# Kernel optimization log

Hardware: AMD Instinct MI355X
Metric: run time of the kernel (lower is better)

Reference implementation:

```python
import jax, jax.numpy as jnp
import numpy as np

N_NODES = 50000
N_EDGES = 800000
N_EVAL = 500000
D = 96


def _sage_conv(x, edge_index, W_l, W_r, b):
    # PyG SAGEConv with aggr='add':
    #   aggr_out[v] = sum_{(u->v) in edges} x[u]
    #   out = aggr_out @ W_l^T-equivalent + b + x @ W_r  (we store W as [in, out])
    src, dst = edge_index[0], edge_index[1]
    msgs = x[src]                                        # [E, d_in] irregular gather
    aggr = jax.ops.segment_sum(msgs, dst, num_segments=x.shape[0])  # [N, d_in]
    return aggr @ W_l + b + x @ W_r                      # [N, d_out]


def setup_inputs() -> dict:
    key = jax.random.key(0)
    ks = jax.random.split(key, 8)
    scale = 1.0 / np.sqrt(D)
    Features = jax.random.normal(ks[0], (N_NODES, D), dtype=jnp.float32)
    A = jax.random.randint(ks[1], (2, N_EDGES), 0, N_NODES, dtype=jnp.int64)
    E = jax.random.randint(ks[2], (2, N_EVAL), 0, N_NODES, dtype=jnp.int64)
    W1_l = jax.random.normal(ks[3], (D, D), dtype=jnp.float32) * scale
    W1_r = jax.random.normal(ks[4], (D, D), dtype=jnp.float32) * scale
    b1 = jnp.zeros((D,), dtype=jnp.float32)
    W2_l = jax.random.normal(ks[5], (D, D), dtype=jnp.float32) * scale
    W2_r = jax.random.normal(ks[6], (D, D), dtype=jnp.float32) * scale
    b2 = jnp.zeros((D,), dtype=jnp.float32)
    return {"Features": Features, "A": A, "E": E,
            "W1_l": W1_l, "W1_r": W1_r, "b1": b1,
            "W2_l": W2_l, "W2_r": W2_r, "b2": b2}


def reference(Features, A, E, W1_l, W1_r, b1, W2_l, W2_r, b2):
    h = _sage_conv(Features, A, W1_l, W1_r, b1)          # [N, hidden]
    h = jax.nn.relu(h)
    # dropout in eval mode = identity
    h = _sage_conv(h, A, W2_l, W2_r, b2)                 # [N, out]
    # edge scoring: gather src/dst embeddings, dot, sigmoid
    src = h[E[0]]                                        # [n_eval, out]
    dst = h[E[1]]                                        # [n_eval, out]
    return jax.nn.sigmoid(jnp.sum(src * dst, axis=-1))   # [n_eval]
```

## Files before the change

### kernel.cpp

```cpp
#include <hip/hip_runtime.h>
#include <math.h>

#define N_NODES 50000
#define N_EDGES 800000
#define N_EVAL  500000
#define SCAN_NB ((N_NODES + 1023) / 1024)
#define CSTRIDE 16

__device__ __forceinline__ float4 f4add(float4 a, float4 b) {
    return make_float4(a.x + b.x, a.y + b.y, a.z + b.z, a.w + b.w);
}
__device__ __forceinline__ float4 f4fma(float s, float4 w, float4 a) {
    return make_float4(fmaf(s, w.x, a.x), fmaf(s, w.y, a.y),
                       fmaf(s, w.z, a.z), fmaf(s, w.w, a.w));
}


__global__ __launch_bounds__(256) void k_rank(const int* __restrict__ dst,
                                              int* __restrict__ degS,
                                              int* __restrict__ rank) {
    int e = blockIdx.x * 256 + threadIdx.x;
    if (e < N_EDGES) {
        int d = dst[e];
        rank[e] = atomicAdd(&degS[(size_t)d * CSTRIDE], 1);
    }
}

__global__ __launch_bounds__(1024) void k_scan1(const int* __restrict__ degS,
                                                int* __restrict__ off,
                                                int* __restrict__ bsum) {
    __shared__ int wsum[16];
    const int idx  = blockIdx.x * 1024 + threadIdx.x;
    const int lane = threadIdx.x & 63;
    const int wid  = threadIdx.x >> 6;
    int v = (idx < N_NODES) ? degS[(size_t)idx * CSTRIDE] : 0;
    int s = v;
    #pragma unroll
    for (int d = 1; d < 64; d <<= 1) {
        int o = __shfl_up(s, (unsigned)d, 64);
        if (lane >= d) s += o;
    }
    if (lane == 63) wsum[wid] = s;
    __syncthreads();
    if (wid == 0) {
        int ws = (lane < 16) ? wsum[lane] : 0;
        #pragma unroll
        for (int d = 1; d < 16; d <<= 1) {
            int o = __shfl_up(ws, (unsigned)d, 64);
            if (lane >= d) ws += o;
        }
        if (lane < 16) wsum[lane] = ws;
    }
    __syncthreads();
    int incl = (wid ? wsum[wid - 1] : 0) + s;
    if (idx < N_NODES) off[idx] = incl - v;
    if (threadIdx.x == 1023) bsum[blockIdx.x] = incl;
}

__global__ __launch_bounds__(64) void k_scan2(int* __restrict__ bsum,
                                              int* __restrict__ off) {
    int lane = threadIdx.x;
    int v = (lane < SCAN_NB) ? bsum[lane] : 0;
    int s = v;
    #pragma unroll
    for (int d = 1; d < 64; d <<= 1) {
        int o = __shfl_up(s, (unsigned)d, 64);
        if (lane >= d) s += o;
    }
    if (lane < SCAN_NB) bsum[lane] = s - v;
    if (lane == 63) off[N_NODES] = s;
}

__global__ __launch_bounds__(1024) void k_scan3(const int* __restrict__ bsum,
                                                int* __restrict__ off) {
    int idx = blockIdx.x * 1024 + threadIdx.x;
    if (idx < N_NODES) off[idx] += bsum[blockIdx.x];
}

__global__ __launch_bounds__(256) void k_fill(const int* __restrict__ src,
                                              const int* __restrict__ dst,
                                              const int* __restrict__ rank,
                                              const int* __restrict__ off,
                                              int* __restrict__ csr) {
    int e = blockIdx.x * 256 + threadIdx.x;
    if (e < N_EDGES) {
        csr[off[dst[e]] + rank[e]] = src[e];
    }
}

__global__ __launch_bounds__(256) void k_aggr(const float* __restrict__ x,
                                              const int* __restrict__ off,
                                              const int* __restrict__ csr,
                                              float* __restrict__ out) {
    int gt = blockIdx.x * 256 + threadIdx.x;
    if (gt >= N_NODES * 24) return;
    int v = gt / 24;
    int c = gt - v * 24;
    const float* xp = x + c * 4;
    int beg = off[v], end = off[v + 1];
    float4 a0 = make_float4(0.f, 0.f, 0.f, 0.f);
    float4 a1 = make_float4(0.f, 0.f, 0.f, 0.f);
    int i = beg;
    for (; i + 8 <= end; i += 8) {
        int u0 = csr[i + 0], u1 = csr[i + 1], u2 = csr[i + 2], u3 = csr[i + 3];
        int u4 = csr[i + 4], u5 = csr[i + 5], u6 = csr[i + 6], u7 = csr[i + 7];
        float4 t0 = *(const float4*)(xp + (size_t)u0 * 96);
        float4 t1 = *(const float4*)(xp + (size_t)u1 * 96);
        float4 t2 = *(const float4*)(xp + (size_t)u2 * 96);
        float4 t3 = *(const float4*)(xp + (size_t)u3 * 96);
        float4 t4 = *(const float4*)(xp + (size_t)u4 * 96);
        float4 t5 = *(const float4*)(xp + (size_t)u5 * 96);
        float4 t6 = *(const float4*)(xp + (size_t)u6 * 96);
        float4 t7 = *(const float4*)(xp + (size_t)u7 * 96);
        a0 = f4add(a0, f4add(f4add(t0, t2), f4add(t4, t6)));
        a1 = f4add(a1, f4add(f4add(t1, t3), f4add(t5, t7)));
    }
    for (; i < end; ++i) {
        int u = csr[i];
        a0 = f4add(a0, *(const float4*)(xp + (size_t)u * 96));
    }
    *(float4*)(out + (size_t)v * 96 + c * 4) = f4add(a0, a1);
}

template <int RELU>
__global__ __launch_bounds__(192) void k_gemm(const float* __restrict__ P,
                                              const float* __restrict__ X,
                                              const float* __restrict__ Wl,
                                              const float* __restrict__ Wr,
                                              const float* __restrict__ bias,
                                              float* __restrict__ out) {
    __shared__ float Ws[32 * 96];
    __shared__ float xT[32 * 68];
    const int tid = threadIdx.x;
    const int q   = tid % 24;
    const int rg  = tid / 24;
    const int v0  = blockIdx.x * 64;

    const int  row0 = tid >> 3,         qd0 = tid & 7;
    const int  row1 = (tid + 192) >> 3, qd1 = (tid + 192) & 7;
    const int  row2 = (tid + 384) >> 3, qd2 = (tid + 384) & 7;
    const bool has2 = (tid < 128);
    int sv0 = v0 + row0; if (sv0 >= N_NODES) sv0 = N_NODES - 1;
    int sv1 = v0 + row1; if (sv1 >= N_NODES) sv1 = N_NODES - 1;
    int sv2 = v0 + row2; if (sv2 >= N_NODES) sv2 = N_NODES - 1;

    float4 bv = *(const float4*)(bias + q * 4);
    float4 acc[8];
    #pragma unroll
    for (int r = 0; r < 8; ++r) acc[r] = make_float4(0.f, 0.f, 0.f, 0.f);

    float4 wreg0, wreg1, wreg2, wreg3;
    float4 xreg0, xreg1, xreg2;

    auto load_chunk = [&](int kc) {
        const float* W = (kc < 3 ? Wl : Wr) + (kc % 3) * (32 * 96);
        const float* M = (kc < 3 ? P : X);
        const int kbase = (kc % 3) * 32;
        wreg0 = *(const float4*)(W + (tid + 0 * 192) * 4);
        wreg1 = *(const float4*)(W + (tid + 1 * 192) * 4);
        wreg2 = *(const float4*)(W + (tid + 2 * 192) * 4);
        wreg3 = *(const float4*)(W + (tid + 3 * 192) * 4);
        xreg0 = *(const float4*)(M + (size_t)sv0 * 96 + kbase + qd0 * 4);
        xreg1 = *(const float4*)(M + (size_t)sv1 * 96 + kbase + qd1 * 4);
        if (has2) xreg2 = *(const float4*)(M + (size_t)sv2 * 96 + kbase + qd2 * 4);
    };
    auto store_chunk = [&]() {
        *(float4*)(Ws + (tid + 0 * 192) * 4) = wreg0;
        *(float4*)(Ws + (tid + 1 * 192) * 4) = wreg1;
        *(float4*)(Ws + (tid + 2 * 192) * 4) = wreg2;
        *(float4*)(Ws + (tid + 3 * 192) * 4) = wreg3;
        int k0 = qd0 * 4;
        xT[(k0 + 0) * 68 + row0] = xreg0.x;
        xT[(k0 + 1) * 68 + row0] = xreg0.y;
        xT[(k0 + 2) * 68 + row0] = xreg0.z;
        xT[(k0 + 3) * 68 + row0] = xreg0.w;
        int k1 = qd1 * 4;
        xT[(k1 + 0) * 68 + row1] = xreg1.x;
        xT[(k1 + 1) * 68 + row1] = xreg1.y;
        xT[(k1 + 2) * 68 + row1] = xreg1.z;
        xT[(k1 + 3) * 68 + row1] = xreg1.w;
        if (has2) {
            int k2 = qd2 * 4;
            xT[(k2 + 0) * 68 + row2] = xreg2.x;
            xT[(k2 + 1) * 68 + row2] = xreg2.y;
            xT[(k2 + 2) * 68 + row2] = xreg2.z;
            xT[(k2 + 3) * 68 + row2] = xreg2.w;
        }
    };

    load_chunk(0);
    for (int kc = 0; kc < 6; ++kc) {
        __syncthreads();
        store_chunk();
        if (kc < 5) load_chunk(kc + 1);
        __syncthreads();
        #pragma unroll 8
        for (int kk = 0; kk < 32; ++kk) {
            float4 w  = *(const float4*)(Ws + kk * 96 + q * 4);
            float4 xa = *(const float4*)(xT + kk * 68 + rg * 8);
            float4 xb = *(const float4*)(xT + kk * 68 + rg * 8 + 4);
            acc[0] = f4fma(xa.x, w, acc[0]);
            acc[1] = f4fma(xa.y, w, acc[1]);
            acc[2] = f4fma(xa.z, w, acc[2]);
            acc[3] = f4fma(xa.w, w, acc[3]);
            acc[4] = f4fma(xb.x, w, acc[4]);
            acc[5] = f4fma(xb.y, w, acc[5]);
            acc[6] = f4fma(xb.z, w, acc[6]);
            acc[7] = f4fma(xb.w, w, acc[7]);
        }
    }
    #pragma unroll
    for (int r = 0; r < 8; ++r) {
        int v = v0 + rg * 8 + r;
        if (v < N_NODES) {
            float4 o = f4add(acc[r], bv);
            if (RELU) {
                o.x = fmaxf(o.x, 0.f); o.y = fmaxf(o.y, 0.f);
                o.z = fmaxf(o.z, 0.f); o.w = fmaxf(o.w, 0.f);
            }
            *(float4*)(out + (size_t)v * 96 + q * 4) = o;
        }
    }
}

__global__ __launch_bounds__(256) void k_score(const float* __restrict__ h,
                                               const int* __restrict__ E,
                                               float* __restrict__ out) {
    int t = blockIdx.x * 256 + threadIdx.x;
    int e = t >> 3, sub = t & 7;
    if (e >= N_EVAL) return;
    int s = E[e];
    int d = E[N_EVAL + e];
    const float* ps = h + (size_t)s * 96 + sub * 12;
    const float* pd = h + (size_t)d * 96 + sub * 12;
    float dot = 0.f;
    #pragma unroll
    for (int i = 0; i < 3; ++i) {
        float4 a = *(const float4*)(ps + i * 4);
        float4 b = *(const float4*)(pd + i * 4);
        dot += a.x * b.x + a.y * b.y + a.z * b.z + a.w * b.w;
    }
    dot += __shfl_xor(dot, 1, 64);
    dot += __shfl_xor(dot, 2, 64);
    dot += __shfl_xor(dot, 4, 64);
    if (sub == 0) out[e] = 1.f / (1.f + expf(-dot));
}


extern "C" void kernel_launch(void* const* d_in, const int* in_sizes, int n_in,
                              void* d_out, int out_size, void* d_ws, size_t ws_size,
                              hipStream_t stream) {
    const float* Features = (const float*)d_in[0];
    const int*   A        = (const int*)d_in[1];
    const int*   E        = (const int*)d_in[2];
    const float* W1l = (const float*)d_in[3];
    const float* W1r = (const float*)d_in[4];
    const float* b1  = (const float*)d_in[5];
    const float* W2l = (const float*)d_in[6];
    const float* W2r = (const float*)d_in[7];
    const float* b2  = (const float*)d_in[8];
    float* out = (float*)d_out;

    char* p = (char*)d_ws;
    auto alloc = [&](size_t bytes) -> char* {
        char* q = p;
        p += (bytes + 255) & ~(size_t)255;
        return q;
    };
    int*   degS = (int*)alloc((size_t)N_NODES * CSTRIDE * 4);
    int*   rank = (int*)alloc((size_t)N_EDGES * 4);
    int*   off  = (int*)alloc((size_t)(N_NODES + 1) * 4);
    int*   bsum = (int*)alloc((size_t)64 * 4);
    int*   csr  = (int*)alloc((size_t)N_EDGES * 4);
    float* bufA = (float*)alloc((size_t)N_NODES * 96 * 4);
    float* bufB = (float*)alloc((size_t)N_NODES * 96 * 4);

    const int* Asrc = A;
    const int* Adst = A + N_EDGES;

    hipMemsetAsync(degS, 0, (size_t)N_NODES * CSTRIDE * 4, stream);
    k_rank<<<(N_EDGES + 255) / 256, 256, 0, stream>>>(Adst, degS, rank);
    k_scan1<<<SCAN_NB, 1024, 0, stream>>>(degS, off, bsum);
    k_scan2<<<1, 64, 0, stream>>>(bsum, off);
    k_scan3<<<SCAN_NB, 1024, 0, stream>>>(bsum, off);
    k_fill<<<(N_EDGES + 255) / 256, 256, 0, stream>>>(Asrc, Adst, rank, off, csr);

    k_aggr<<<(N_NODES * 24 + 255) / 256, 256, 0, stream>>>(Features, off, csr, bufA);
    k_gemm<1><<<(N_NODES + 63) / 64, 192, 0, stream>>>(bufA, Features, W1l, W1r, b1, bufB);

    k_aggr<<<(N_NODES * 24 + 255) / 256, 256, 0, stream>>>(bufB, off, csr, bufA);
    k_gemm<0><<<(N_NODES + 63) / 64, 192, 0, stream>>>(bufA, bufB, W2l, W2r, b2, bufA);

    k_score<<<(N_EVAL * 8 + 255) / 256, 256, 0, stream>>>(bufA, E, out);
}
```

Before: 334.9 us.

## Fuse neighbor aggregation into SAGE GEMM kernel via shared-memory staging

Merges the separate aggregation and GEMM kernels into one kernel per layer. Each 64-node block gathers and sums its neighbor features straight into a transposed shared-memory tile, then multiplies by W_l, then loads its own rows for W_r. This removes the intermediate aggregated buffer's global write and read and one launch per layer. In exchange, the gather phase runs with only 192 threads per block, uses more shared memory (which lowers occupancy), and loses the register prefetch pipelining the GEMM had, so gather latency may be harder to hide.

```diff
diff --git a/kernel.cpp b/kernel.cpp
--- a/kernel.cpp
+++ b/kernel.cpp
@@ -88,117 +88,76 @@
     }
 }
 
-__global__ __launch_bounds__(256) void k_aggr(const float* __restrict__ x,
-                                              const int* __restrict__ off,
-                                              const int* __restrict__ csr,
-                                              float* __restrict__ out) {
-    int gt = blockIdx.x * 256 + threadIdx.x;
-    if (gt >= N_NODES * 24) return;
-    int v = gt / 24;
-    int c = gt - v * 24;
-    const float* xp = x + c * 4;
-    int beg = off[v], end = off[v + 1];
-    float4 a0 = make_float4(0.f, 0.f, 0.f, 0.f);
-    float4 a1 = make_float4(0.f, 0.f, 0.f, 0.f);
-    int i = beg;
-    for (; i + 8 <= end; i += 8) {
-        int u0 = csr[i + 0], u1 = csr[i + 1], u2 = csr[i + 2], u3 = csr[i + 3];
-        int u4 = csr[i + 4], u5 = csr[i + 5], u6 = csr[i + 6], u7 = csr[i + 7];
-        float4 t0 = *(const float4*)(xp + (size_t)u0 * 96);
-        float4 t1 = *(const float4*)(xp + (size_t)u1 * 96);
-        float4 t2 = *(const float4*)(xp + (size_t)u2 * 96);
-        float4 t3 = *(const float4*)(xp + (size_t)u3 * 96);
-        float4 t4 = *(const float4*)(xp + (size_t)u4 * 96);
-        float4 t5 = *(const float4*)(xp + (size_t)u5 * 96);
-        float4 t6 = *(const float4*)(xp + (size_t)u6 * 96);
-        float4 t7 = *(const float4*)(xp + (size_t)u7 * 96);
-        a0 = f4add(a0, f4add(f4add(t0, t2), f4add(t4, t6)));
-        a1 = f4add(a1, f4add(f4add(t1, t3), f4add(t5, t7)));
-    }
-    for (; i < end; ++i) {
-        int u = csr[i];
-        a0 = f4add(a0, *(const float4*)(xp + (size_t)u * 96));
-    }
-    *(float4*)(out + (size_t)v * 96 + c * 4) = f4add(a0, a1);
-}
-
 template <int RELU>
-__global__ __launch_bounds__(192) void k_gemm(const float* __restrict__ P,
-                                              const float* __restrict__ X,
-                                              const float* __restrict__ Wl,
-                                              const float* __restrict__ Wr,
-                                              const float* __restrict__ bias,
-                                              float* __restrict__ out) {
+__global__ __launch_bounds__(192) void k_aggemm(const float* __restrict__ X,
+                                                const int* __restrict__ off,
+                                                const int* __restrict__ csr,
+                                                const float* __restrict__ Wl,
+                                                const float* __restrict__ Wr,
+                                                const float* __restrict__ bias,
+                                                float* __restrict__ out) {
     __shared__ float Ws[32 * 96];
-    __shared__ float xT[32 * 68];
+    __shared__ float U[96 * 68];
     const int tid = threadIdx.x;
-    const int q   = tid % 24;
-    const int rg  = tid / 24;
     const int v0  = blockIdx.x * 64;
 
-    const int  row0 = tid >> 3,         qd0 = tid & 7;
-    const int  row1 = (tid + 192) >> 3, qd1 = (tid + 192) & 7;
-    const int  row2 = (tid + 384) >> 3, qd2 = (tid + 384) & 7;
-    const bool has2 = (tid < 128);
-    int sv0 = v0 + row0; if (sv0 >= N_NODES) sv0 = N_NODES - 1;
-    int sv1 = v0 + row1; if (sv1 >= N_NODES) sv1 = N_NODES - 1;
-    int sv2 = v0 + row2; if (sv2 >= N_NODES) sv2 = N_NODES - 1;
-
+    {
+        const int s = tid / 24;
+        const int c = tid % 24;
+        const float* xp = X + c * 4;
+        for (int r = 0; r < 8; ++r) {
+            const int n = r * 8 + s;
+            const int v = v0 + n;
+            float4 a0 = make_float4(0.f, 0.f, 0.f, 0.f);
+            float4 a1 = make_float4(0.f, 0.f, 0.f, 0.f);
+            if (v < N_NODES) {
+                int beg = off[v], end = off[v + 1];
+                int i = beg;
+                for (; i + 4 <= end; i += 4) {
+                    int u0 = csr[i + 0], u1 = csr[i + 1];
+                    int u2 = csr[i + 2], u3 = csr[i + 3];
+                    float4 t0 = *(const float4*)(xp + (size_t)u0 * 96);
+                    float4 t1 = *(const float4*)(xp + (size_t)u1 * 96);
+                    float4 t2 = *(const float4*)(xp + (size_t)u2 * 96);
+                    float4 t3 = *(const float4*)(xp + (size_t)u3 * 96);
+                    a0 = f4add(a0, f4add(t0, t2));
+                    a1 = f4add(a1, f4add(t1, t3));
+                }
+                for (; i < end; ++i)
+                    a0 = f4add(a0, *(const float4*)(xp + (size_t)csr[i] * 96));
+            }
+            a0 = f4add(a0, a1);
+            const int k0 = c * 4;
+            U[(k0 + 0) * 68 + n] = a0.x;
+            U[(k0 + 1) * 68 + n] = a0.y;
+            U[(k0 + 2) * 68 + n] = a0.z;
+            U[(k0 + 3) * 68 + n] = a0.w;
+        }
+    }
+
+    const int q  = tid % 24;
+    const int rg = tid / 24;
     float4 bv = *(const float4*)(bias + q * 4);
     float4 acc[8];
     #pragma unroll
     for (int r = 0; r < 8; ++r) acc[r] = make_float4(0.f, 0.f, 0.f, 0.f);
 
-    float4 wreg0, wreg1, wreg2, wreg3;
-    float4 xreg0, xreg1, xreg2;
-
-    auto load_chunk = [&](int kc) {
-        const float* W = (kc < 3 ? Wl : Wr) + (kc % 3) * (32 * 96);
-        const float* M = (kc < 3 ? P : X);
-        const int kbase = (kc % 3) * 32;
-        wreg0 = *(const float4*)(W + (tid + 0 * 192) * 4);
-        wreg1 = *(const float4*)(W + (tid + 1 * 192) * 4);
-        wreg2 = *(const float4*)(W + (tid + 2 * 192) * 4);
-        wreg3 = *(const float4*)(W + (tid + 3 * 192) * 4);
-        xreg0 = *(const float4*)(M + (size_t)sv0 * 96 + kbase + qd0 * 4);
-        xreg1 = *(const float4*)(M + (size_t)sv1 * 96 + kbase + qd1 * 4);
-        if (has2) xreg2 = *(const float4*)(M + (size_t)sv2 * 96 + kbase + qd2 * 4);
-    };
-    auto store_chunk = [&]() {
-        *(float4*)(Ws + (tid + 0 * 192) * 4) = wreg0;
-        *(float4*)(Ws + (tid + 1 * 192) * 4) = wreg1;
-        *(float4*)(Ws + (tid + 2 * 192) * 4) = wreg2;
-        *(float4*)(Ws + (tid + 3 * 192) * 4) = wreg3;
-        int k0 = qd0 * 4;
-        xT[(k0 + 0) * 68 + row0] = xreg0.x;
-        xT[(k0 + 1) * 68 + row0] = xreg0.y;
-        xT[(k0 + 2) * 68 + row0] = xreg0.z;
-        xT[(k0 + 3) * 68 + row0] = xreg0.w;
-        int k1 = qd1 * 4;
-        xT[(k1 + 0) * 68 + row1] = xreg1.x;
-        xT[(k1 + 1) * 68 + row1] = xreg1.y;
-        xT[(k1 + 2) * 68 + row1] = xreg1.z;
-        xT[(k1 + 3) * 68 + row1] = xreg1.w;
-        if (has2) {
-            int k2 = qd2 * 4;
-            xT[(k2 + 0) * 68 + row2] = xreg2.x;
-            xT[(k2 + 1) * 68 + row2] = xreg2.y;
-            xT[(k2 + 2) * 68 + row2] = xreg2.z;
-            xT[(k2 + 3) * 68 + row2] = xreg2.w;
-        }
-    };
-
-    load_chunk(0);
-    for (int kc = 0; kc < 6; ++kc) {
+    __syncthreads();
+
+    for (int kc = 0; kc < 3; ++kc) {
+        if (kc) __syncthreads();
+        const float* W = Wl + kc * (32 * 96);
+        #pragma unroll
+        for (int i2 = 0; i2 < 4; ++i2)
+            *(float4*)(Ws + (tid + i2 * 192) * 4) =
+                *(const float4*)(W + (tid + i2 * 192) * 4);
         __syncthreads();
-        store_chunk();
-        if (kc < 5) load_chunk(kc + 1);
-        __syncthreads();
+        const float* Ub = U + kc * 32 * 68;
         #pragma unroll 8
         for (int kk = 0; kk < 32; ++kk) {
             float4 w  = *(const float4*)(Ws + kk * 96 + q * 4);
-            float4 xa = *(const float4*)(xT + kk * 68 + rg * 8);
-            float4 xb = *(const float4*)(xT + kk * 68 + rg * 8 + 4);
+            float4 xa = *(const float4*)(Ub + kk * 68 + rg * 8);
+            float4 xb = *(const float4*)(Ub + kk * 68 + rg * 8 + 4);
             acc[0] = f4fma(xa.x, w, acc[0]);
             acc[1] = f4fma(xa.y, w, acc[1]);
             acc[2] = f4fma(xa.z, w, acc[2]);
@@ -209,6 +168,63 @@
             acc[7] = f4fma(xb.w, w, acc[7]);
         }
     }
+
+    const int  row0 = tid >> 3,         qd0 = tid & 7;
+    const int  row1 = (tid + 192) >> 3, qd1 = (tid + 192) & 7;
+    const int  row2 = (tid + 384) >> 3, qd2 = (tid + 384) & 7;
+    const bool has2 = (tid < 128);
+    int sv0 = v0 + row0; if (sv0 >= N_NODES) sv0 = N_NODES - 1;
+    int sv1 = v0 + row1; if (sv1 >= N_NODES) sv1 = N_NODES - 1;
+    int sv2 = v0 + row2; if (sv2 >= N_NODES) sv2 = N_NODES - 1;
+
+    for (int kc = 0; kc < 3; ++kc) {
+        __syncthreads();
+        const float* W = Wr + kc * (32 * 96);
+        const int kbase = kc * 32;
+        #pragma unroll
+        for (int i2 = 0; i2 < 4; ++i2)
+            *(float4*)(Ws + (tid + i2 * 192) * 4) =
+                *(const float4*)(W + (tid + i2 * 192) * 4);
+        float4 x0 = *(const float4*)(X + (size_t)sv0 * 96 + kbase + qd0 * 4);
+        float4 x1 = *(const float4*)(X + (size_t)sv1 * 96 + kbase + qd1 * 4);
+        float4 x2 = make_float4(0.f, 0.f, 0.f, 0.f);
+        if (has2) x2 = *(const float4*)(X + (size_t)sv2 * 96 + kbase + qd2 * 4);
+        {
+            int k0 = qd0 * 4;
+            U[(k0 + 0) * 68 + row0] = x0.x;
+            U[(k0 + 1) * 68 + row0] = x0.y;
+            U[(k0 + 2) * 68 + row0] = x0.z;
+            U[(k0 + 3) * 68 + row0] = x0.w;
+            int k1 = qd1 * 4;
+            U[(k1 + 0) * 68 + row1] = x1.x;
+            U[(k1 + 1) * 68 + row1] = x1.y;
+            U[(k1 + 2) * 68 + row1] = x1.z;
+            U[(k1 + 3) * 68 + row1] = x1.w;
+            if (has2) {
+                int k2 = qd2 * 4;
+                U[(k2 + 0) * 68 + row2] = x2.x;
+                U[(k2 + 1) * 68 + row2] = x2.y;
+                U[(k2 + 2) * 68 + row2] = x2.z;
+                U[(k2 + 3) * 68 + row2] = x2.w;
+            }
+        }
+        __syncthreads();
+        #pragma unroll 8
+        for (int kk = 0; kk < 32; ++kk) {
+            float4 w  = *(const float4*)(Ws + kk * 96 + q * 4);
+            float4 xa = *(const float4*)(U + kk * 68 + rg * 8);
+            float4 xb = *(const float4*)(U + kk * 68 + rg * 8 + 4);
+            acc[0] = f4fma(xa.x, w, acc[0]);
+            acc[1] = f4fma(xa.y, w, acc[1]);
+            acc[2] = f4fma(xa.z, w, acc[2]);
+            acc[3] = f4fma(xa.w, w, acc[3]);
+            acc[4] = f4fma(xb.x, w, acc[4]);
+            acc[5] = f4fma(xb.y, w, acc[5]);
+            acc[6] = f4fma(xb.z, w, acc[6]);
+            acc[7] = f4fma(xb.w, w, acc[7]);
+        }
+    }
+
     #pragma unroll
     for (int r = 0; r < 8; ++r) {
         int v = v0 + rg * 8 + r;
@@ -285,11 +301,10 @@
     k_scan3<<<SCAN_NB, 1024, 0, stream>>>(bsum, off);
     k_fill<<<(N_EDGES + 255) / 256, 256, 0, stream>>>(Asrc, Adst, rank, off, csr);
 
-    k_aggr<<<(N_NODES * 24 + 255) / 256, 256, 0, stream>>>(Features, off, csr, bufA);
-    k_gemm<1><<<(N_NODES + 63) / 64, 192, 0, stream>>>(bufA, Features, W1l, W1r, b1, bufB);
-
-    k_aggr<<<(N_NODES * 24 + 255) / 256, 256, 0, stream>>>(bufB, off, csr, bufA);
-    k_gemm<0><<<(N_NODES + 63) / 64, 192, 0, stream>>>(bufA, bufB, W2l, W2r, b2, bufA);
+    k_aggemm<1><<<(N_NODES + 63) / 64, 192, 0, stream>>>(Features, off, csr,
+                                                         W1l, W1r, b1, bufB);
+    k_aggemm<0><<<(N_NODES + 63) / 64, 192, 0, stream>>>(bufB, off, csr,
+                                                         W2l, W2r, b2, bufA);
 
     k_score<<<(N_EVAL * 8 + 255) / 256, 256, 0, stream>>>(bufA, E, out);
 }
```

New measurement: 410.8 us. 1.23x slower.
